# Kernel optimization log

Hardware: AMD Instinct MI355X
Metric: run time of the kernel (lower is better)

## Reference

```python
import jax, jax.numpy as jnp
import numpy as np

D = 1024
H = 4
HD = D // H
B = 256
L = 64
DILATIONS = (1, 4, 8, 16)


def setup_inputs() -> dict:
    key = jax.random.key(0)
    ks = jax.random.split(key, 12)
    s = 1.0 / np.sqrt(D)
    return {
        "x": jax.random.normal(ks[0], (B, D), jnp.float32),
        "hist": jax.random.normal(ks[1], (L, B, D), jnp.float32),
        "Wq": jax.random.normal(ks[2], (D, D), jnp.float32) * s,
        "bq": jnp.zeros((D,), jnp.float32),
        "Wk": jax.random.normal(ks[3], (D, D), jnp.float32) * s,
        "bk": jnp.zeros((D,), jnp.float32),
        "Wv": jax.random.normal(ks[4], (D, D), jnp.float32) * s,
        "bv": jnp.zeros((D,), jnp.float32),
        "Wo": jax.random.normal(ks[5], (D, D), jnp.float32) * s,
        "bo": jnp.zeros((D,), jnp.float32),
        "dil_w": jnp.full((len(DILATIONS),), 1.0 / len(DILATIONS), jnp.float32),
        "gamma": jnp.ones((D,), jnp.float32),
        "beta": jnp.zeros((D,), jnp.float32),
    }


def reference(x, hist, Wq, bq, Wk, bk, Wv, bv, Wo, bo, dil_w, gamma, beta):
    scale = 1.0 / np.sqrt(HD)
    q = (x @ Wq + bq).reshape(B, H, HD)  # (B, H, HD)
    attended = []
    for d in DILATIONS:
        # history frames at stride d, concatenated along dim 0 (faithful to torch.cat)
        frames = hist[::d].reshape(-1, D)              # (T', D), T' = ceil(L/d)*B
        k = (frames @ Wk + bk).reshape(-1, H, HD)      # (T', H, HD)
        v = (frames @ Wv + bv).reshape(-1, H, HD)
        s = jnp.einsum('bhd,thd->bht', q, k) * scale   # (B, H, T')
        a = jax.nn.softmax(s, axis=-1)
        attended.append(jnp.einsum('bht,thd->bhd', a, v).reshape(B, D))
    w = jax.nn.softmax(dil_w, axis=0)
    combined = sum(w[i] * attended[i] for i in range(len(DILATIONS)))
    y = x + combined @ Wo + bo
    mu = jnp.mean(y, axis=-1, keepdims=True)
    var = jnp.var(y, axis=-1, keepdims=True)
    return (y - mu) / jnp.sqrt(var + 1e-5) * gamma + beta
```

## Files before the change

kernel.cpp:

```cpp
#include <hip/hip_runtime.h>


#define DD    1024
#define TALL  16384

typedef _Float16 half8  __attribute__((ext_vector_type(8)));
typedef _Float16 half4v __attribute__((ext_vector_type(4)));
typedef float    floatx4 __attribute__((ext_vector_type(4)));
typedef unsigned int u32;

static const size_t OFF_WOT  = 0;
static const size_t OFF_WV16 = 2097152;
static const size_t OFF_WK16 = 4194304;
static const size_t OFF_WQ16 = 6291456;
static const size_t OFF_XB   = 8388608;
static const size_t OFF_G    = 8912896;
static const size_t OFF_WVOT = 11010048;
static const size_t OFF_WQKT = 19398656;
static const size_t OFF_BVWO = 27787264;
static const size_t OFF_BQK  = 27791360;
static const size_t OFF_PHR  = 27807744;
static const size_t OFF_OPP  = 29904896;
static const size_t OFF_HB   = 38293504;
static const size_t OFF_HT   = 71848960;
static const size_t OFF_S    = 105403392;

__device__ __forceinline__ size_t chunk16_off(int g) {
  if (g < 4)  return (size_t)g * 2097152;
  if (g < 8)  return 19398656 + (size_t)(g - 4) * 2097152;
  if (g < 12) return 29904896 + (size_t)(g - 8) * 2097152;
  return 38293504 + (size_t)(g - 12) * 2097152;
}

__device__ __forceinline__ void gl_lds16(const void* g, void* l) {
  __builtin_amdgcn_global_load_lds((const __attribute__((address_space(1))) u32*)g,
                                   (__attribute__((address_space(3))) u32*)l, 16, 0, 0);
}

__global__ void prep_kernel(const float* __restrict__ Wo, const float* __restrict__ Wv,
                            const float* __restrict__ Wk, const float* __restrict__ Wq,
                            const float* __restrict__ x, const float* __restrict__ hist,
                            _Float16* __restrict__ WoT, _Float16* __restrict__ Wv16,
                            _Float16* __restrict__ Wk16, _Float16* __restrict__ Wq16,
                            _Float16* __restrict__ xb, _Float16* __restrict__ histb,
                            _Float16* __restrict__ histT) {
  int bid = blockIdx.x, tid = threadIdx.x;
  if (bid < 1024) {
    int k0 = (bid & 31) * 32, n0 = (bid >> 5) * 32;
    __shared__ float t32[32][33];
    int tx = tid & 31, ty = tid >> 5;
#pragma unroll
    for (int i = 0; i < 4; i++) {
      int r = ty + i * 8;
      t32[r][tx] = Wo[(size_t)(k0 + r) * DD + n0 + tx];
    }
    __syncthreads();
#pragma unroll
    for (int i = 0; i < 4; i++) {
      int r = ty + i * 8;
      WoT[(size_t)(n0 + r) * DD + k0 + tx] = (_Float16)t32[tx][r];
    }
  } else if (bid < 4352) {
    const float* src; _Float16* dst; size_t i;
    if (bid < 2048)      { src = Wv; dst = Wv16; i = (size_t)(bid - 1024) * 256 + tid; }
    else if (bid < 3072) { src = Wk; dst = Wk16; i = (size_t)(bid - 2048) * 256 + tid; }
    else if (bid < 4096) { src = Wq; dst = Wq16; i = (size_t)(bid - 3072) * 256 + tid; }
    else                 { src = x;  dst = xb;   i = (size_t)(bid - 4096) * 256 + tid; }
    float4 v = ((const float4*)src)[i];
    half4v h = {(_Float16)v.x, (_Float16)v.y, (_Float16)v.z, (_Float16)v.w};
    *(half4v*)(dst + 4 * i) = h;
  } else {
    int tb = bid - 4352;
    int t0 = (tb & 255) * 64, f0 = (tb >> 8) * 64;
    __shared__ _Float16 lt[64][72];
    int r = tid >> 2, c0 = (tid & 3) * 16;
    half8 s0, s1;
#pragma unroll
    for (int i = 0; i < 4; i++) {
      float4 v = *(const float4*)&hist[(size_t)(t0 + r) * 1024 + f0 + c0 + i * 4];
      half4v h = {(_Float16)v.x, (_Float16)v.y, (_Float16)v.z, (_Float16)v.w};
      *(half4v*)&lt[r][c0 + i * 4] = h;
      if (i < 2) { s0[i*4]=h[0]; s0[i*4+1]=h[1]; s0[i*4+2]=h[2]; s0[i*4+3]=h[3]; }
      else { s1[(i-2)*4]=h[0]; s1[(i-2)*4+1]=h[1]; s1[(i-2)*4+2]=h[2]; s1[(i-2)*4+3]=h[3]; }
    }
    *(half8*)&histb[(size_t)(t0 + r) * 1024 + f0 + c0] = s0;
    *(half8*)&histb[(size_t)(t0 + r) * 1024 + f0 + c0 + 8] = s1;
    __syncthreads();
    int fr = tid >> 2, tc0 = (tid & 3) * 16;
    half8 o0, o1;
#pragma unroll
    for (int j = 0; j < 8; j++) { o0[j] = lt[tc0 + j][fr]; o1[j] = lt[tc0 + 8 + j][fr]; }
    *(half8*)&histT[(size_t)(f0 + fr) * TALL + t0 + tc0] = o0;
    *(half8*)&histT[(size_t)(f0 + fr) * TALL + t0 + tc0 + 8] = o1;
  }
}

__device__ __forceinline__ void gemm_core(const _Float16* __restrict__ A, size_t lda,
                                          const _Float16* __restrict__ B, size_t ldb,
                                          int kIters, _Float16* As, _Float16* Bs,
                                          int tid, floatx4 acc[4][4]) {
  int lane = tid & 63, w = tid >> 6;
  int l15 = lane & 15, quad = lane >> 4;
  int wm = (w >> 1) * 64, wn = (w & 1) * 64;
  int swz = ((tid & 3) ^ ((tid >> 3) & 3)) * 8;
  int pch = (quad ^ ((l15 >> 1) & 3)) * 8;
  const char* gA0 = (const char*)(A + (size_t)(tid >> 2) * lda + swz);
  const char* gA1 = (const char*)(A + ((size_t)(tid >> 2) + 64) * lda + swz);
  const char* gB0 = (const char*)(B + (size_t)(tid >> 2) * ldb + swz);
  const char* gB1 = (const char*)(B + ((size_t)(tid >> 2) + 64) * ldb + swz);
  _Float16* lA = As + w * 512;
  _Float16* lB = Bs + w * 512;
#define GC_STAGE(buf, k)                                    \
  do {                                                      \
    size_t off_ = (size_t)(k) * 64;                         \
    gl_lds16(gA0 + off_, lA + (buf) * 4096);                \
    gl_lds16(gA1 + off_, lA + (buf) * 4096 + 2048);         \
    gl_lds16(gB0 + off_, lB + (buf) * 4096);                \
    gl_lds16(gB1 + off_, lB + (buf) * 4096 + 2048);         \
  } while (0)
#define GC_STEP(buf, k)                                                       \
  do {                                                                        \
    if ((k) + 1 < kIters) asm volatile("s_waitcnt vmcnt(4)" ::: "memory");    \
    else                  asm volatile("s_waitcnt vmcnt(0)" ::: "memory");    \
    asm volatile("s_barrier" ::: "memory");                                   \
    const _Float16* Ac_ = As + (buf) * 4096;                                  \
    const _Float16* Bc_ = Bs + (buf) * 4096;                                  \
    half8 a_[4];                                                              \
    _Pragma("unroll")                                                         \
    for (int mi = 0; mi < 4; mi++)                                            \
      a_[mi] = *(const half8*)&Ac_[(wm + mi * 16 + l15) * 32 + pch];          \
    _Pragma("unroll")                                                         \
    for (int ni = 0; ni < 4; ni++) {                                          \
      half8 b8_ = *(const half8*)&Bc_[(wn + ni * 16 + l15) * 32 + pch];       \
      _Pragma("unroll")                                                       \
      for (int mi = 0; mi < 4; mi++)                                          \
        acc[mi][ni] = __builtin_amdgcn_mfma_f32_16x16x32_f16(a_[mi], b8_,     \
                                                             acc[mi][ni], 0, 0, 0); \
    }                                                                         \
    asm volatile("s_waitcnt lgkmcnt(0)" ::: "memory");                        \
    asm volatile("s_barrier" ::: "memory");                                   \
    if ((k) + 2 < kIters) GC_STAGE(buf, (k) + 2);                             \
  } while (0)
  GC_STAGE(0, 0);
  GC_STAGE(1, 1);
  for (int kk = 0; kk < kIters; kk += 2) {
    GC_STEP(0, kk);
    GC_STEP(1, kk + 1);
  }
#undef GC_STEP
#undef GC_STAGE
}

__device__ __forceinline__ void gemm256_core(const _Float16* __restrict__ A, size_t lda,
                                             const _Float16* __restrict__ B, size_t ldb,
                                             int nT, _Float16* As, _Float16* Bs,
                                             int tid, floatx4 acc[8][4]) {
  int lane = tid & 63, w = tid >> 6;
  int l15 = lane & 15, quad = lane >> 4;
  int wr = w >> 2, wc = w & 3;
  int pch = (quad ^ ((l15 >> 1) & 3)) * 8;
  int srow = tid >> 2;
  int schunk = (tid & 3) ^ ((tid >> 3) & 3);
  const char* gA0 = (const char*)(A + (size_t)srow * lda + schunk * 8);
  const char* gA1 = (const char*)(A + (size_t)(srow + 128) * lda + schunk * 8);
  const char* gB0 = (const char*)(B + (size_t)srow * ldb + schunk * 8);
  const char* gB1 = (const char*)(B + (size_t)(srow + 128) * ldb + schunk * 8);
  _Float16* lA = As + w * 512;
  _Float16* lB = Bs + w * 512;
#define STA256(buf, t)                                        \
  do { size_t o_ = (size_t)(t) * 64;                          \
    gl_lds16(gA0 + o_, lA + (buf) * 8192);                    \
    gl_lds16(gA1 + o_, lA + (buf) * 8192 + 4096);             \
  } while (0)
#define STB256(buf, t)                                        \
  do { size_t o_ = (size_t)(t) * 64;                          \
    gl_lds16(gB0 + o_, lB + (buf) * 8192);                    \
    gl_lds16(gB1 + o_, lB + (buf) * 8192 + 4096);             \
  } while (0)
  STA256(0, 0); STB256(0, 0);
  if (nT > 1) { STA256(1, 1); STB256(1, 1); }
  if (nT > 2) { STA256(2, 2); STB256(2, 2); }
  for (int t = 0; t < nT; ++t) {
    int buf = t & 3;
    if (t + 2 < nT)      asm volatile("s_waitcnt vmcnt(8)" ::: "memory");
    else if (t + 1 < nT) asm volatile("s_waitcnt vmcnt(4)" ::: "memory");
    else                 asm volatile("s_waitcnt vmcnt(0)" ::: "memory");
    asm volatile("s_barrier" ::: "memory");
    const _Float16* Ac = As + buf * 8192;
    const _Float16* Bc = Bs + buf * 8192;
    half8 b8[4], a8[4];
#pragma unroll
    for (int ni = 0; ni < 4; ni++)
      b8[ni] = *(const half8*)&Bc[(wc * 64 + ni * 16 + l15) * 32 + pch];
#pragma unroll
    for (int mi = 0; mi < 4; mi++)
      a8[mi] = *(const half8*)&Ac[(wr * 128 + mi * 16 + l15) * 32 + pch];
    if (t + 3 < nT) STA256((t + 3) & 3, t + 3);
    asm volatile("s_barrier" ::: "memory");
    asm volatile("s_waitcnt lgkmcnt(0)" ::: "memory");
    __builtin_amdgcn_s_setprio(1);
#pragma unroll
    for (int mi = 0; mi < 4; mi++)
#pragma unroll
      for (int ni = 0; ni < 4; ni++)
        acc[mi][ni] = __builtin_amdgcn_mfma_f32_16x16x32_f16(a8[mi], b8[ni], acc[mi][ni], 0, 0, 0);
    __builtin_amdgcn_s_setprio(0);
    asm volatile("s_barrier" ::: "memory");
#pragma unroll
    for (int mi = 0; mi < 4; mi++)
      a8[mi] = *(const half8*)&Ac[(wr * 128 + 64 + mi * 16 + l15) * 32 + pch];
    if (t + 3 < nT) STB256((t + 3) & 3, t + 3);
    asm volatile("s_barrier" ::: "memory");
    asm volatile("s_waitcnt lgkmcnt(0)" ::: "memory");
    __builtin_amdgcn_s_setprio(1);
#pragma unroll
    for (int mi = 0; mi < 4; mi++)
#pragma unroll
      for (int ni = 0; ni < 4; ni++)
        acc[4 + mi][ni] = __builtin_amdgcn_mfma_f32_16x16x32_f16(a8[mi], b8[ni], acc[4 + mi][ni], 0, 0, 0);
    __builtin_amdgcn_s_setprio(0);
    asm volatile("s_barrier" ::: "memory");
  }
#undef STA256
#undef STB256
}

template <bool OUTF32>
__launch_bounds__(256, 3)
__global__ void gemm_f16_kernel(const _Float16* __restrict__ A, size_t lda, size_t aoffz,
                                const _Float16* __restrict__ B, size_t ldb, size_t boffz,
                                int kIters, const float* __restrict__ bias, size_t biasoffz,
                                float scale, void* __restrict__ C, size_t ldc, size_t coffz) {
  __shared__ __align__(16) _Float16 As[8192];
  __shared__ __align__(16) _Float16 Bs[8192];
  int tid = threadIdx.x;
  const _Float16* Ab = A + aoffz * blockIdx.z + (size_t)(blockIdx.y * 128) * lda;
  const _Float16* Bb = B + boffz * blockIdx.z + (size_t)(blockIdx.x * 128) * ldb;
  floatx4 acc[4][4];
  floatx4 zero = {0.f, 0.f, 0.f, 0.f};
#pragma unroll
  for (int a = 0; a < 4; a++)
#pragma unroll
    for (int b = 0; b < 4; b++) acc[a][b] = zero;
  gemm_core(Ab, lda, Bb, ldb, kIters, As, Bs, tid, acc);
  int lane = tid & 63, w = tid >> 6;
  int l15 = lane & 15, quad = lane >> 4;
  int wm = (w >> 1) * 64, wn = (w & 1) * 64;
#pragma unroll
  for (int mi = 0; mi < 4; mi++)
#pragma unroll
    for (int ni = 0; ni < 4; ni++) {
      int colg = blockIdx.x * 128 + wn + ni * 16 + l15;
      float bv = bias ? bias[biasoffz * blockIdx.z + colg] : 0.f;
#pragma unroll
      for (int r = 0; r < 4; r++) {
        int rowg = blockIdx.y * 128 + wm + mi * 16 + quad * 4 + r;
        float v = (acc[mi][ni][r] + bv) * scale;
        size_t idx = coffz * blockIdx.z + (size_t)rowg * ldc + colg;
        if (OUTF32) ((float*)C)[idx] = v;
        else ((_Float16*)C)[idx] = (_Float16)v;
      }
    }
}

__launch_bounds__(256, 3)
__global__ void wpack_kernel(const _Float16* __restrict__ WoT, const _Float16* __restrict__ Wv16,
                             const _Float16* __restrict__ Wk16, const _Float16* __restrict__ Wq16,
                             const float* __restrict__ bv, const float* __restrict__ bq,
                             _Float16* __restrict__ WVOT, _Float16* __restrict__ WQKT,
                             float* __restrict__ bvwo, float* __restrict__ bqk) {
  __shared__ __align__(16) _Float16 As[8192];
  __shared__ __align__(16) _Float16 Bs[8192];
  int bid = blockIdx.x, tid = threadIdx.x;
  if (bid < 512) {
    bool isQK = bid >= 256;
    int g = bid & 255;
    int x = g & 7, y = (g >> 3) & 7, z = g >> 6;
    const _Float16* A = isQK ? Wk16 : WoT;
    const _Float16* B = isQK ? Wq16 : Wv16;
    const _Float16* Ab = A + 256 * z + (size_t)(y * 128) * 1024;
    const _Float16* Bb = B + 256 * z + (size_t)(x * 128) * 1024;
    floatx4 acc[4][4];
    floatx4 zero = {0.f, 0.f, 0.f, 0.f};
#pragma unroll
    for (int a = 0; a < 4; a++)
#pragma unroll
      for (int b = 0; b < 4; b++) acc[a][b] = zero;
    gemm_core(Ab, 1024, Bb, 1024, 8, As, Bs, tid, acc);
    float scale = isQK ? 0.0625f : 1.0f;
    _Float16* C = isQK ? WQKT : WVOT;
    size_t ldc = isQK ? 1024 : 4096;
    size_t zoff = isQK ? (size_t)1048576 * z : (size_t)1024 * z;
    int lane = tid & 63, w = tid >> 6;
    int l15 = lane & 15, quad = lane >> 4;
    int wm = (w >> 1) * 64, wn = (w & 1) * 64;
#pragma unroll
    for (int mi = 0; mi < 4; mi++)
#pragma unroll
      for (int ni = 0; ni < 4; ni++) {
        int col = x * 128 + wn + ni * 16 + l15;
#pragma unroll
        for (int r = 0; r < 4; r++) {
          int row = y * 128 + wm + mi * 16 + quad * 4 + r;
          C[zoff + (size_t)row * ldc + col] = (_Float16)(acc[mi][ni][r] * scale);
        }
      }
  } else if (bid < 516) {
    int j = (bid - 512) * 256 + tid;
    const half8* row = (const half8*)(WoT + (size_t)j * 1024);
    float a = 0.f;
    for (int c = 0; c < 128; c++) {
      half8 w8 = row[c];
#pragma unroll
      for (int e = 0; e < 8; e++) a += bv[c * 8 + e] * (float)w8[e];
    }
    bvwo[j] = a;
  } else {
    int idx = (bid - 516) * 256 + tid;
    int h = idx >> 10, f = idx & 1023;
    const _Float16* row = Wk16 + (size_t)f * 1024 + h * 256;
    float a = 0.f;
    for (int n = 0; n < 256; n++) a += bq[h * 256 + n] * (float)row[n];
    bqk[idx] = a * 0.0625f;
  }
}

__launch_bounds__(512, 2)
__global__ void gemm256_s_kernel(const _Float16* __restrict__ G, const _Float16* __restrict__ histb,
                                 _Float16* __restrict__ Eout, float* __restrict__ zframe) {
  __shared__ __align__(16) _Float16 SM[65536];
  _Float16* As = SM;
  _Float16* Bs = SM + 32768;
  int bid = blockIdx.x, tid = threadIdx.x;
  int h = bid >> 6, nt = bid & 63;
  const _Float16* Ab = G + (size_t)h * 262144;
  const _Float16* Bb = histb + (size_t)(nt * 256) * 1024;
  floatx4 acc[8][4];
  floatx4 zero = {0.f, 0.f, 0.f, 0.f};
#pragma unroll
  for (int a = 0; a < 8; a++)
#pragma unroll
    for (int b = 0; b < 4; b++) acc[a][b] = zero;
  gemm256_core(Ab, 1024, Bb, 1024, 32, As, Bs, tid, acc);
  int lane = tid & 63, w = tid >> 6;
  int l15 = lane & 15, quad = lane >> 4;
  int wr = w >> 2, wc = w & 3;
  __syncthreads();
#pragma unroll
  for (int mh = 0; mh < 2; mh++)
#pragma unroll
    for (int mi = 0; mi < 4; mi++)
#pragma unroll
      for (int ni = 0; ni < 4; ni++) {
        int col = wc * 64 + ni * 16 + l15;
#pragma unroll
        for (int r = 0; r < 4; r++) {
          int row = wr * 128 + mh * 64 + mi * 16 + quad * 4 + r;
          SM[row * 256 + col] = (_Float16)__expf(acc[mh * 4 + mi][ni][r]);
        }
      }
  __syncthreads();
  int c32 = lane & 31, hs = lane >> 5;
#pragma unroll
  for (int it = 0; it < 16; it++) {
    int row = w * 32 + it * 2 + hs;
    half8 v = *(const half8*)&SM[row * 256 + c32 * 8];
    float s = 0.f;
#pragma unroll
    for (int j = 0; j < 8; j++) s += (float)v[j];
#pragma unroll
    for (int off = 1; off <= 16; off <<= 1) s += __shfl_xor(s, off, 64);
    *(half8*)&Eout[(size_t)h * 4194304 + (size_t)row * TALL + nt * 256 + c32 * 8] = v;
    if (c32 == 0) zframe[(size_t)(h * 256 + row) * 64 + nt] = s;
  }
}

__global__ void csoftmax_kernel(const float* __restrict__ zframe, const float* __restrict__ dil_w,
                                float* __restrict__ ctab) {
  int row = blockIdx.x * 256 + threadIdx.x;
  const float* z = zframe + (size_t)row * 64;
  float z1 = 0.f, z4 = 0.f, z8 = 0.f, z16 = 0.f;
#pragma unroll
  for (int f = 0; f < 64; f++) {
    float v = z[f];
    z1 += v;
    if (!(f & 3))  z4 += v;
    if (!(f & 7))  z8 += v;
    if (!(f & 15)) z16 += v;
  }
  float w0 = dil_w[0], w1 = dil_w[1], w2 = dil_w[2], w3 = dil_w[3];
  float wmx = fmaxf(fmaxf(w0, w1), fmaxf(w2, w3));
  float e0 = __expf(w0 - wmx), e1 = __expf(w1 - wmx), e2 = __expf(w2 - wmx), e3 = __expf(w3 - wmx);
  float wsum = e0 + e1 + e2 + e3;
  float b0 = (e0 / wsum) / z1 * 256.0f;
  float b1 = (e1 / wsum) / z4 * 256.0f;
  float b2 = (e2 / wsum) / z8 * 256.0f;
  float b3 = (e3 / wsum) / z16 * 256.0f;
  float* c = ctab + (size_t)row * 64;
#pragma unroll
  for (int f = 0; f < 64; f++) {
    float cv = b0;
    if (!(f & 3))  cv += b1;
    if (!(f & 7))  cv += b2;
    if (!(f & 15)) cv += b3;
    c[f] = cv;
  }
}

__launch_bounds__(512, 2)
__global__ void gemm256_ph_kernel(const _Float16* __restrict__ E, const _Float16* __restrict__ histT,
                                  const float* __restrict__ ctab, char* __restrict__ ws) {
  __shared__ __align__(16) _Float16 SM[65536];
  _Float16* As = SM;
  _Float16* Bs = SM + 16384;
  int bid = blockIdx.x, tid = threadIdx.x;
  int xcd = bid & 7, slot = bid >> 3;
  int g = xcd + 8 * (slot >> 4);
  int member = slot & 15;
  int h = member >> 2, nt = member & 3;
  int lane = tid & 63, w = tid >> 6;
  int l15 = lane & 15, quad = lane >> 4;
  int wr = w >> 2, wc = w & 3;
  int pch = (quad ^ ((l15 >> 1) & 3)) * 8;
  int srow = tid >> 2;
  int schunk = (tid & 3) ^ ((tid >> 3) & 3);
  const _Float16* gA = E + (size_t)h * 4194304 + (size_t)g * 1024 + (size_t)srow * TALL + schunk * 8;
  const _Float16* gB = histT + (size_t)(nt * 256) * TALL + (size_t)g * 1024 + (size_t)srow * TALL + schunk * 8;
  const float* cr0 = ctab + (size_t)(h * 256 + srow) * 64 + g * 4;
  const float* cr1 = cr0 + (size_t)128 * 64;
  _Float16* lA = As + w * 512 + lane * 8;
  _Float16* lB = Bs + w * 512 + lane * 8;
  floatx4 acc[8][4];
  floatx4 zero = {0.f, 0.f, 0.f, 0.f};
#pragma unroll
  for (int a = 0; a < 8; a++)
#pragma unroll
    for (int b = 0; b < 4; b++) acc[a][b] = zero;
  half8 xa0, xa1, xb0, xb1; float xc0, xc1;
  half8 ya0, ya1, yb0, yb1; float yc0, yc1;
#define PH_LOAD(P, t)                                                         \
  do { size_t o_ = (size_t)(t) * 32;                                          \
    P##a0 = *(const half8*)(gA + o_);                                         \
    P##a1 = *(const half8*)(gA + o_ + (size_t)128 * TALL);                    \
    P##b0 = *(const half8*)(gB + o_);                                         \
    P##b1 = *(const half8*)(gB + o_ + (size_t)128 * TALL);                    \
    P##c0 = cr0[(t) >> 3]; P##c1 = cr1[(t) >> 3];                             \
  } while (0)
#define PH_COMPUTE(b)                                                         \
  do {                                                                        \
    const _Float16* Ac_ = As + (b) * 8192;                                    \
    const _Float16* Bc_ = Bs + (b) * 8192;                                    \
    half8 bb_[4], aa_[4];                                                     \
    _Pragma("unroll")                                                         \
    for (int ni = 0; ni < 4; ni++)                                            \
      bb_[ni] = *(const half8*)&Bc_[(wc * 64 + ni * 16 + l15) * 32 + pch];    \
    _Pragma("unroll")                                                         \
    for (int mi = 0; mi < 4; mi++)                                            \
      aa_[mi] = *(const half8*)&Ac_[(wr * 128 + mi * 16 + l15) * 32 + pch];   \
    __builtin_amdgcn_s_setprio(1);                                            \
    _Pragma("unroll")                                                         \
    for (int mi = 0; mi < 4; mi++) {                                          \
      _Pragma("unroll")                                                       \
      for (int ni = 0; ni < 4; ni++)                                          \
        acc[mi][ni] = __builtin_amdgcn_mfma_f32_16x16x32_f16(aa_[mi], bb_[ni], acc[mi][ni], 0, 0, 0); \
    }                                                                         \
    __builtin_amdgcn_s_setprio(0);                                            \
    _Pragma("unroll")                                                         \
    for (int mi = 0; mi < 4; mi++)                                            \
      aa_[mi] = *(const half8*)&Ac_[(wr * 128 + 64 + mi * 16 + l15) * 32 + pch]; \
    __builtin_amdgcn_s_setprio(1);                                            \
    _Pragma("unroll")                                                         \
    for (int mi = 0; mi < 4; mi++) {                                          \
      _Pragma("unroll")                                                       \
      for (int ni = 0; ni < 4; ni++)                                          \
        acc[4 + mi][ni] = __builtin_amdgcn_mfma_f32_16x16x32_f16(aa_[mi], bb_[ni], acc[4 + mi][ni], 0, 0, 0); \
    }                                                                         \
    __builtin_amdgcn_s_setprio(0);                                            \
  } while (0)
#define PH_STEP(P, N, t, b)                                                   \
  do {                                                                        \
    if ((t) + 1 < 32) PH_LOAD(N, (t) + 1);                                    \
    _Float16 ch0_ = (_Float16)P##c0, ch1_ = (_Float16)P##c1;                  \
    half8 w0_, w1_;                                                           \
    _Pragma("unroll")                                                         \
    for (int j = 0; j < 8; j++) { w0_[j] = P##a0[j] * ch0_; w1_[j] = P##a1[j] * ch1_; } \
    *(half8*)(lA + (b) * 8192) = w0_;                                         \
    *(half8*)(lA + (b) * 8192 + 4096) = w1_;                                  \
    *(half8*)(lB + (b) * 8192) = P##b0;                                       \
    *(half8*)(lB + (b) * 8192 + 4096) = P##b1;                                \
    asm volatile("s_waitcnt lgkmcnt(0)" ::: "memory");                        \
    asm volatile("s_barrier" ::: "memory");                                   \
    PH_COMPUTE(b);                                                            \
    asm volatile("s_waitcnt lgkmcnt(0)" ::: "memory");                        \
    asm volatile("s_barrier" ::: "memory");                                   \
  } while (0)
  PH_LOAD(x, 0);
  for (int t = 0; t < 32; t += 2) {
    PH_STEP(x, y, t, 0);
    PH_STEP(y, x, t + 1, 1);
  }
#undef PH_STEP
#undef PH_COMPUTE
#undef PH_LOAD
  __syncthreads();
#pragma unroll
  for (int mh = 0; mh < 2; mh++)
#pragma unroll
    for (int mi = 0; mi < 4; mi++)
#pragma unroll
      for (int ni = 0; ni < 4; ni++) {
        int col = wc * 64 + ni * 16 + l15;
#pragma unroll
        for (int r = 0; r < 4; r++) {
          int row = wr * 128 + mh * 64 + mi * 16 + quad * 4 + r;
          SM[row * 256 + col] = (_Float16)acc[mh * 4 + mi][ni][r];
        }
      }
  __syncthreads();
  _Float16* chunk = (_Float16*)(ws + chunk16_off(g));
  int c32 = lane & 31, hs = lane >> 5;
  int colbase = h * 1024 + nt * 256;
#pragma unroll
  for (int it = 0; it < 16; it++) {
    int row = w * 32 + it * 2 + hs;
    half8 v = *(const half8*)&SM[row * 256 + c32 * 8];
    *(half8*)&chunk[(size_t)row * 4096 + colbase + c32 * 8] = v;
  }
}

__global__ void reduce_ph_kernel(const char* __restrict__ ws, _Float16* __restrict__ PHred) {
  size_t e8 = ((size_t)blockIdx.x * 256 + threadIdx.x) * 8;
  float s[8] = {0.f, 0.f, 0.f, 0.f, 0.f, 0.f, 0.f, 0.f};
#pragma unroll
  for (int g = 0; g < 16; g++) {
    const _Float16* p = (const _Float16*)(ws + chunk16_off(g));
    half8 v = *(const half8*)&p[e8];
#pragma unroll
    for (int j = 0; j < 8; j++) s[j] += (float)v[j];
  }
  half8 o;
#pragma unroll
  for (int j = 0; j < 8; j++) o[j] = (_Float16)s[j];
  *(half8*)&PHred[e8] = o;
}

__global__ void ln_kernel(const float* __restrict__ x, const float* __restrict__ part2,
                          const float* __restrict__ bo, const float* __restrict__ bvwo,
                          const float* __restrict__ gamma, const float* __restrict__ beta,
                          float* __restrict__ out) {
  int b = blockIdx.x, t = threadIdx.x;
  __shared__ float red[8];
  float y[4];
  float sum = 0.f, sq = 0.f;
#pragma unroll
  for (int i = 0; i < 4; i++) {
    int j = t + i * 256;
    float v = x[(size_t)b * 1024 + j] + bo[j] + bvwo[j];
#pragma unroll
    for (int z = 0; z < 8; z++) v += part2[(size_t)z * 262144 + (size_t)b * 1024 + j];
    y[i] = v;
    sum += v;
    sq += v * v;
  }
#pragma unroll
  for (int off = 1; off < 64; off <<= 1) {
    sum += __shfl_xor(sum, off, 64);
    sq += __shfl_xor(sq, off, 64);
  }
  int w = t >> 6, lane = t & 63;
  if (lane == 0) { red[w] = sum; red[4 + w] = sq; }
  __syncthreads();
  sum = red[0] + red[1] + red[2] + red[3];
  sq = red[4] + red[5] + red[6] + red[7];
  float mu = sum * (1.f / 1024.f);
  float var = sq * (1.f / 1024.f) - mu * mu;
  float inv = rsqrtf(var + 1e-5f);
#pragma unroll
  for (int i = 0; i < 4; i++) {
    int j = t + i * 256;
    out[(size_t)b * 1024 + j] = (y[i] - mu) * inv * gamma[j] + beta[j];
  }
}

extern "C" void kernel_launch(void* const* d_in, const int* in_sizes, int n_in,
                              void* d_out, int out_size, void* d_ws, size_t ws_size,
                              hipStream_t stream) {
  const float* x     = (const float*)d_in[0];
  const float* hist  = (const float*)d_in[1];
  const float* Wq    = (const float*)d_in[2];
  const float* bq    = (const float*)d_in[3];
  const float* Wk    = (const float*)d_in[4];
  const float* Wv    = (const float*)d_in[6];
  const float* bv    = (const float*)d_in[7];
  const float* Wo    = (const float*)d_in[8];
  const float* bo    = (const float*)d_in[9];
  const float* dil_w = (const float*)d_in[10];
  const float* gamma = (const float*)d_in[11];
  const float* beta  = (const float*)d_in[12];
  char* ws = (char*)d_ws;

  _Float16* WoT   = (_Float16*)(ws + OFF_WOT);
  _Float16* Wv16  = (_Float16*)(ws + OFF_WV16);
  _Float16* Wk16  = (_Float16*)(ws + OFF_WK16);
  _Float16* Wq16  = (_Float16*)(ws + OFF_WQ16);
  _Float16* xb    = (_Float16*)(ws + OFF_XB);
  _Float16* G     = (_Float16*)(ws + OFF_G);
  _Float16* WVOT  = (_Float16*)(ws + OFF_WVOT);
  _Float16* WQKT  = (_Float16*)(ws + OFF_WQKT);
  float* bvwo     = (float*)(ws + OFF_BVWO);
  float* bqk      = (float*)(ws + OFF_BQK);
  _Float16* PHred = (_Float16*)(ws + OFF_PHR);
  float* oppart   = (float*)(ws + OFF_OPP);
  _Float16* histb = (_Float16*)(ws + OFF_HB);
  _Float16* histT = (_Float16*)(ws + OFF_HT);
  _Float16* Eb    = (_Float16*)(ws + OFF_S);
  float* zframe   = (float*)(ws + OFF_WQKT);
  float* ctab     = (float*)(ws + OFF_G);

  prep_kernel<<<dim3(8448), 256, 0, stream>>>(Wo, Wv, Wk, Wq, x, hist,
                                              WoT, Wv16, Wk16, Wq16, xb, histb, histT);
  wpack_kernel<<<dim3(532), 256, 0, stream>>>(WoT, Wv16, Wk16, Wq16, bv, bq,
                                              WVOT, WQKT, bvwo, bqk);
  gemm_f16_kernel<false><<<dim3(8, 2, 4), 256, 0, stream>>>(
      xb, 1024, 0, WQKT, 1024, 1048576, 32, bqk, 1024, 1.0f, (void*)G, 1024, 262144);
  gemm256_s_kernel<<<dim3(256), 512, 0, stream>>>(G, histb, Eb, zframe);
  csoftmax_kernel<<<dim3(4), 256, 0, stream>>>(zframe, dil_w, ctab);
  gemm256_ph_kernel<<<dim3(256), 512, 0, stream>>>(Eb, histT, ctab, ws);
  reduce_ph_kernel<<<dim3(512), 256, 0, stream>>>(ws, PHred);
  gemm_f16_kernel<true><<<dim3(8, 2, 8), 256, 0, stream>>>(
      PHred, 4096, 512, WVOT, 4096, 512, 16, nullptr, 0, 1.0f / 256.0f,
      (void*)oppart, 1024, 262144);
  ln_kernel<<<dim3(256), 256, 0, stream>>>(x, oppart, bo, bvwo, gamma, beta, (float*)d_out);
}
```

Baseline: 323.4 us.

## Regroup frames by dilation weight class and stream PH tiles via direct LDS loads

```diff
diff --git a/kernel.cpp b/kernel.cpp
--- a/kernel.cpp
+++ b/kernel.cpp
@@ -30,6 +30,16 @@
   if (g < 8)  return 19398656 + (size_t)(g - 4) * 2097152;
   if (g < 12) return 29904896 + (size_t)(g - 8) * 2097152;
   return 38293504 + (size_t)(g - 12) * 2097152;
+}
+
+__device__ __forceinline__ int frame_of(int g, int j) {
+  if (g < 12) { int m = g * 4 + j; return m + m / 3 + 1; }
+  if (g < 14) return 4 + 8 * ((g - 12) * 4 + j);
+  if (g == 14) return 8 + 16 * j;
+  return 16 * j;
+}
+__device__ __forceinline__ size_t foff(int g, int t) {
+  return (size_t)frame_of(g, t >> 3) * 512 + (size_t)(t & 7) * 64;
 }
 
 __device__ __forceinline__ void gl_lds16(const void* g, void* l) {
@@ -356,7 +366,8 @@
 #pragma unroll
         for (int r = 0; r < 4; r++) {
           int row = wr * 128 + mh * 64 + mi * 16 + quad * 4 + r;
-          SM[row * 256 + col] = (_Float16)__expf(acc[mh * 4 + mi][ni][r]);
+          int colsw = col ^ (((row >> 2) & 3) << 3);
+          SM[row * 256 + colsw] = (_Float16)__expf(acc[mh * 4 + mi][ni][r]);
         }
       }
   __syncthreads();
@@ -364,7 +375,8 @@
 #pragma unroll
   for (int it = 0; it < 16; it++) {
     int row = w * 32 + it * 2 + hs;
-    half8 v = *(const half8*)&SM[row * 256 + c32 * 8];
+    int cs = (c32 * 8) ^ (((row >> 2) & 3) << 3);
+    half8 v = *(const half8*)&SM[row * 256 + cs];
     float s = 0.f;
 #pragma unroll
     for (int j = 0; j < 8; j++) s += (float)v[j];
@@ -376,7 +388,7 @@
 }
 
 __global__ void csoftmax_kernel(const float* __restrict__ zframe, const float* __restrict__ dil_w,
-                                float* __restrict__ ctab) {
+                                float* __restrict__ w4) {
   int row = blockIdx.x * 256 + threadIdx.x;
   const float* z = zframe + (size_t)row * 64;
   float z1 = 0.f, z4 = 0.f, z8 = 0.f, z16 = 0.f;
@@ -396,23 +408,19 @@
   float b1 = (e1 / wsum) / z4 * 256.0f;
   float b2 = (e2 / wsum) / z8 * 256.0f;
   float b3 = (e3 / wsum) / z16 * 256.0f;
-  float* c = ctab + (size_t)row * 64;
-#pragma unroll
-  for (int f = 0; f < 64; f++) {
-    float cv = b0;
-    if (!(f & 3))  cv += b1;
-    if (!(f & 7))  cv += b2;
-    if (!(f & 15)) cv += b3;
-    c[f] = cv;
-  }
+  float* wr = w4 + (size_t)row * 4;
+  wr[0] = b0;
+  wr[1] = b0 + b1;
+  wr[2] = b0 + b1 + b2;
+  wr[3] = b0 + b1 + b2 + b3;
 }
 
 __launch_bounds__(512, 2)
 __global__ void gemm256_ph_kernel(const _Float16* __restrict__ E, const _Float16* __restrict__ histT,
-                                  const float* __restrict__ ctab, char* __restrict__ ws) {
+                                  char* __restrict__ ws) {
   __shared__ __align__(16) _Float16 SM[65536];
   _Float16* As = SM;
-  _Float16* Bs = SM + 16384;
+  _Float16* Bs = SM + 32768;
   int bid = blockIdx.x, tid = threadIdx.x;
   int xcd = bid & 7, slot = bid >> 3;
   int g = xcd + 8 * (slot >> 4);
@@ -424,84 +432,76 @@
   int pch = (quad ^ ((l15 >> 1) & 3)) * 8;
   int srow = tid >> 2;
   int schunk = (tid & 3) ^ ((tid >> 3) & 3);
-  const _Float16* gA = E + (size_t)h * 4194304 + (size_t)g * 1024 + (size_t)srow * TALL + schunk * 8;
-  const _Float16* gB = histT + (size_t)(nt * 256) * TALL + (size_t)g * 1024 + (size_t)srow * TALL + schunk * 8;
-  const float* cr0 = ctab + (size_t)(h * 256 + srow) * 64 + g * 4;
-  const float* cr1 = cr0 + (size_t)128 * 64;
-  _Float16* lA = As + w * 512 + lane * 8;
-  _Float16* lB = Bs + w * 512 + lane * 8;
+  const _Float16* A = E + (size_t)h * 4194304;
+  const _Float16* B = histT + (size_t)(nt * 256) * TALL;
+  const char* gA0 = (const char*)(A + (size_t)srow * TALL + schunk * 8);
+  const char* gA1 = (const char*)(A + (size_t)(srow + 128) * TALL + schunk * 8);
+  const char* gB0 = (const char*)(B + (size_t)srow * TALL + schunk * 8);
+  const char* gB1 = (const char*)(B + (size_t)(srow + 128) * TALL + schunk * 8);
+  _Float16* lA = As + w * 512;
+  _Float16* lB = Bs + w * 512;
   floatx4 acc[8][4];
   floatx4 zero = {0.f, 0.f, 0.f, 0.f};
 #pragma unroll
   for (int a = 0; a < 8; a++)
 #pragma unroll
     for (int b = 0; b < 4; b++) acc[a][b] = zero;
-  half8 xa0, xa1, xb0, xb1; float xc0, xc1;
-  half8 ya0, ya1, yb0, yb1; float yc0, yc1;
-#define PH_LOAD(P, t)                                                         \
-  do { size_t o_ = (size_t)(t) * 32;                                          \
-    P##a0 = *(const half8*)(gA + o_);                                         \
-    P##a1 = *(const half8*)(gA + o_ + (size_t)128 * TALL);                    \
-    P##b0 = *(const half8*)(gB + o_);                                         \
-    P##b1 = *(const half8*)(gB + o_ + (size_t)128 * TALL);                    \
-    P##c0 = cr0[(t) >> 3]; P##c1 = cr1[(t) >> 3];                             \
+#define PSTA(buf, t)                                          \
+  do { size_t o_ = foff(g, t);                                \
+    gl_lds16(gA0 + o_, lA + (buf) * 8192);                    \
+    gl_lds16(gA1 + o_, lA + (buf) * 8192 + 4096);             \
   } while (0)
-#define PH_COMPUTE(b)                                                         \
-  do {                                                                        \
-    const _Float16* Ac_ = As + (b) * 8192;                                    \
-    const _Float16* Bc_ = Bs + (b) * 8192;                                    \
-    half8 bb_[4], aa_[4];                                                     \
-    _Pragma("unroll")                                                         \
-    for (int ni = 0; ni < 4; ni++)                                            \
-      bb_[ni] = *(const half8*)&Bc_[(wc * 64 + ni * 16 + l15) * 32 + pch];    \
-    _Pragma("unroll")                                                         \
-    for (int mi = 0; mi < 4; mi++)                                            \
-      aa_[mi] = *(const half8*)&Ac_[(wr * 128 + mi * 16 + l15) * 32 + pch];   \
-    __builtin_amdgcn_s_setprio(1);                                            \
-    _Pragma("unroll")                                                         \
-    for (int mi = 0; mi < 4; mi++) {                                          \
-      _Pragma("unroll")                                                       \
-      for (int ni = 0; ni < 4; ni++)                                          \
-        acc[mi][ni] = __builtin_amdgcn_mfma_f32_16x16x32_f16(aa_[mi], bb_[ni], acc[mi][ni], 0, 0, 0); \
-    }                                                                         \
-    __builtin_amdgcn_s_setprio(0);                                            \
-    _Pragma("unroll")                                                         \
-    for (int mi = 0; mi < 4; mi++)                                            \
-      aa_[mi] = *(const half8*)&Ac_[(wr * 128 + 64 + mi * 16 + l15) * 32 + pch]; \
-    __builtin_amdgcn_s_setprio(1);                                            \
-    _Pragma("unroll")                                                         \
-    for (int mi = 0; mi < 4; mi++) {                                          \
-      _Pragma("unroll")                                                       \
-      for (int ni = 0; ni < 4; ni++)                                          \
-        acc[4 + mi][ni] = __builtin_amdgcn_mfma_f32_16x16x32_f16(aa_[mi], bb_[ni], acc[4 + mi][ni], 0, 0, 0); \
-    }                                                                         \
-    __builtin_amdgcn_s_setprio(0);                                            \
+#define PSTB(buf, t)                                          \
+  do { size_t o_ = foff(g, t);                                \
+    gl_lds16(gB0 + o_, lB + (buf) * 8192);                    \
+    gl_lds16(gB1 + o_, lB + (buf) * 8192 + 4096);             \
   } while (0)
-#define PH_STEP(P, N, t, b)                                                   \
-  do {                                                                        \
-    if ((t) + 1 < 32) PH_LOAD(N, (t) + 1);                                    \
-    _Float16 ch0_ = (_Float16)P##c0, ch1_ = (_Float16)P##c1;                  \
-    half8 w0_, w1_;                                                           \
-    _Pragma("unroll")                                                         \
-    for (int j = 0; j < 8; j++) { w0_[j] = P##a0[j] * ch0_; w1_[j] = P##a1[j] * ch1_; } \
-    *(half8*)(lA + (b) * 8192) = w0_;                                         \
-    *(half8*)(lA + (b) * 8192 + 4096) = w1_;                                  \
-    *(half8*)(lB + (b) * 8192) = P##b0;                                       \
-    *(half8*)(lB + (b) * 8192 + 4096) = P##b1;                                \
-    asm volatile("s_waitcnt lgkmcnt(0)" ::: "memory");                        \
-    asm volatile("s_barrier" ::: "memory");                                   \
-    PH_COMPUTE(b);                                                            \
-    asm volatile("s_waitcnt lgkmcnt(0)" ::: "memory");                        \
-    asm volatile("s_barrier" ::: "memory");                                   \
-  } while (0)
-  PH_LOAD(x, 0);
-  for (int t = 0; t < 32; t += 2) {
-    PH_STEP(x, y, t, 0);
-    PH_STEP(y, x, t + 1, 1);
-  }
-#undef PH_STEP
-#undef PH_COMPUTE
-#undef PH_LOAD
+  PSTA(0, 0); PSTB(0, 0);
+  PSTA(1, 1); PSTB(1, 1);
+  PSTA(2, 2); PSTB(2, 2);
+  for (int t = 0; t < 32; ++t) {
+    int buf = t & 3;
+    if (t + 2 < 32)      asm volatile("s_waitcnt vmcnt(8)" ::: "memory");
+    else if (t + 1 < 32) asm volatile("s_waitcnt vmcnt(4)" ::: "memory");
+    else                 asm volatile("s_waitcnt vmcnt(0)" ::: "memory");
+    asm volatile("s_barrier" ::: "memory");
+    const _Float16* Ac = As + buf * 8192;
+    const _Float16* Bc = Bs + buf * 8192;
+    half8 b8[4], a8[4];
+#pragma unroll
+    for (int ni = 0; ni < 4; ni++)
+      b8[ni] = *(const half8*)&Bc[(wc * 64 + ni * 16 + l15) * 32 + pch];
+#pragma unroll
+    for (int mi = 0; mi < 4; mi++)
+      a8[mi] = *(const half8*)&Ac[(wr * 128 + mi * 16 + l15) * 32 + pch];
+    if (t + 3 < 32) PSTA((t + 3) & 3, t + 3);
+    asm volatile("s_barrier" ::: "memory");
+    asm volatile("s_waitcnt lgkmcnt(0)" ::: "memory");
+    __builtin_amdgcn_s_setprio(1);
+#pragma unroll
+    for (int mi = 0; mi < 4; mi++)
+#pragma unroll
+      for (int ni = 0; ni < 4; ni++)
+        acc[mi][ni] = __builtin_amdgcn_mfma_f32_16x16x32_f16(a8[mi], b8[ni], acc[mi][ni], 0, 0, 0);
+    __builtin_amdgcn_s_setprio(0);
+    asm volatile("s_barrier" ::: "memory");
+#pragma unroll
+    for (int mi = 0; mi < 4; mi++)
+      a8[mi] = *(const half8*)&Ac[(wr * 128 + 64 + mi * 16 + l15) * 32 + pch];
+    if (t + 3 < 32) PSTB((t + 3) & 3, t + 3);
+    asm volatile("s_barrier" ::: "memory");
+    asm volatile("s_waitcnt lgkmcnt(0)" ::: "memory");
+    __builtin_amdgcn_s_setprio(1);
+#pragma unroll
+    for (int mi = 0; mi < 4; mi++)
+#pragma unroll
+      for (int ni = 0; ni < 4; ni++)
+        acc[4 + mi][ni] = __builtin_amdgcn_mfma_f32_16x16x32_f16(a8[mi], b8[ni], acc[4 + mi][ni], 0, 0, 0);
+    __builtin_amdgcn_s_setprio(0);
+    asm volatile("s_barrier" ::: "memory");
+  }
+#undef PSTA
+#undef PSTB
   __syncthreads();
 #pragma unroll
   for (int mh = 0; mh < 2; mh++)
@@ -513,7 +513,8 @@
 #pragma unroll
         for (int r = 0; r < 4; r++) {
           int row = wr * 128 + mh * 64 + mi * 16 + quad * 4 + r;
-          SM[row * 256 + col] = (_Float16)acc[mh * 4 + mi][ni][r];
+          int colsw = col ^ (((row >> 2) & 3) << 3);
+          SM[row * 256 + colsw] = (_Float16)acc[mh * 4 + mi][ni][r];
         }
       }
   __syncthreads();
@@ -523,24 +524,51 @@
 #pragma unroll
   for (int it = 0; it < 16; it++) {
     int row = w * 32 + it * 2 + hs;
-    half8 v = *(const half8*)&SM[row * 256 + c32 * 8];
+    int cs = (c32 * 8) ^ (((row >> 2) & 3) << 3);
+    half8 v = *(const half8*)&SM[row * 256 + cs];
     *(half8*)&chunk[(size_t)row * 4096 + colbase + c32 * 8] = v;
   }
 }
 
-__global__ void reduce_ph_kernel(const char* __restrict__ ws, _Float16* __restrict__ PHred) {
+__global__ void reduce_ph_kernel(const char* __restrict__ ws, const float* __restrict__ w4,
+                                 _Float16* __restrict__ PHred) {
   size_t e8 = ((size_t)blockIdx.x * 256 + threadIdx.x) * 8;
-  float s[8] = {0.f, 0.f, 0.f, 0.f, 0.f, 0.f, 0.f, 0.f};
-#pragma unroll
-  for (int g = 0; g < 16; g++) {
+  int q = (int)(e8 >> 12);
+  int h = (int)((e8 >> 10) & 3);
+  const float* wr = w4 + (size_t)(h * 256 + q) * 4;
+  float sA[8] = {0,0,0,0,0,0,0,0}, sB[8] = {0,0,0,0,0,0,0,0};
+  float sC[8] = {0,0,0,0,0,0,0,0}, sD[8] = {0,0,0,0,0,0,0,0};
+#pragma unroll
+  for (int g = 0; g < 12; g++) {
     const _Float16* p = (const _Float16*)(ws + chunk16_off(g));
     half8 v = *(const half8*)&p[e8];
 #pragma unroll
-    for (int j = 0; j < 8; j++) s[j] += (float)v[j];
-  }
+    for (int j = 0; j < 8; j++) sA[j] += (float)v[j];
+  }
+#pragma unroll
+  for (int g = 12; g < 14; g++) {
+    const _Float16* p = (const _Float16*)(ws + chunk16_off(g));
+    half8 v = *(const half8*)&p[e8];
+#pragma unroll
+    for (int j = 0; j < 8; j++) sB[j] += (float)v[j];
+  }
+  {
+    const _Float16* p = (const _Float16*)(ws + chunk16_off(14));
+    half8 v = *(const half8*)&p[e8];
+#pragma unroll
+    for (int j = 0; j < 8; j++) sC[j] += (float)v[j];
+  }
+  {
+    const _Float16* p = (const _Float16*)(ws + chunk16_off(15));
+    half8 v = *(const half8*)&p[e8];
+#pragma unroll
+    for (int j = 0; j < 8; j++) sD[j] += (float)v[j];
+  }
+  float wA = wr[0], wB = wr[1], wC = wr[2], wD = wr[3];
   half8 o;
 #pragma unroll
-  for (int j = 0; j < 8; j++) o[j] = (_Float16)s[j];
+  for (int j = 0; j < 8; j++)
+    o[j] = (_Float16)(wA * sA[j] + wB * sB[j] + wC * sC[j] + wD * sD[j]);
   *(half8*)&PHred[e8] = o;
 }
 
@@ -615,7 +643,7 @@
   _Float16* histT = (_Float16*)(ws + OFF_HT);
   _Float16* Eb    = (_Float16*)(ws + OFF_S);
   float* zframe   = (float*)(ws + OFF_WQKT);
-  float* ctab     = (float*)(ws + OFF_G);
+  float* w4       = (float*)(ws + OFF_G);
 
   prep_kernel<<<dim3(8448), 256, 0, stream>>>(Wo, Wv, Wk, Wq, x, hist,
                                               WoT, Wv16, Wk16, Wq16, xb, histb, histT);
@@ -624,9 +652,9 @@
   gemm_f16_kernel<false><<<dim3(8, 2, 4), 256, 0, stream>>>(
       xb, 1024, 0, WQKT, 1024, 1048576, 32, bqk, 1024, 1.0f, (void*)G, 1024, 262144);
   gemm256_s_kernel<<<dim3(256), 512, 0, stream>>>(G, histb, Eb, zframe);
-  csoftmax_kernel<<<dim3(4), 256, 0, stream>>>(zframe, dil_w, ctab);
-  gemm256_ph_kernel<<<dim3(256), 512, 0, stream>>>(Eb, histT, ctab, ws);
-  reduce_ph_kernel<<<dim3(512), 256, 0, stream>>>(ws, PHred);
+  csoftmax_kernel<<<dim3(4), 256, 0, stream>>>(zframe, dil_w, w4);
+  gemm256_ph_kernel<<<dim3(256), 512, 0, stream>>>(Eb, histT, ws);
+  reduce_ph_kernel<<<dim3(512), 256, 0, stream>>>(ws, w4, PHred);
   gemm_f16_kernel<true><<<dim3(8, 2, 8), 256, 0, stream>>>(
       PHred, 4096, 512, WVOT, 4096, 512, 16, nullptr, 0, 1.0f / 256.0f,
       (void*)oppart, 1024, 262144);
```

Measured after the change: 309.7 us. -4.2%, faster.
